# Optimization experiments

Hardware: AMD Instinct MI355X
Metric: run time of the kernel (lower is better)

## Reference

```python
import jax, jax.numpy as jnp
import numpy as np

V, E, HID, D = 10000, 512, 512, 14
FEAT = 512  # attention feature dim (== C)


def setup_inputs() -> dict:
    key = jax.random.key(0)
    ks = jax.random.split(key, 20)
    s = 0.02
    inp = {
        "features": jax.random.normal(ks[0], (32, 512, 7, 7), jnp.float32),
        "captions": jax.random.randint(ks[1], (32, 60), 0, V),
        "disease": jax.random.uniform(ks[2], (32, D), jnp.float32),
        # embedding
        "emb": jax.random.normal(ks[3], (V, E), jnp.float32) * s,
        # attention: attn Linear(feat+hid -> hid), v Linear(hid -> 1)
        "W_attn": jax.random.normal(ks[4], (FEAT + HID, HID), jnp.float32) * s,
        "b_attn": jnp.zeros((HID,), jnp.float32),
        "W_v": jax.random.normal(ks[5], (HID, 1), jnp.float32) * s,
        "b_v": jnp.zeros((1,), jnp.float32),
        # attention disease_proj: 14->128->512
        "W_dp1": jax.random.normal(ks[6], (D, 128), jnp.float32) * s,
        "b_dp1": jnp.zeros((128,), jnp.float32),
        "W_dp2": jax.random.normal(ks[7], (128, HID), jnp.float32) * s,
        "b_dp2": jnp.zeros((HID,), jnp.float32),
        # disease_encoder: 14->128->256 (dropout = identity at eval)
        "W_de1": jax.random.normal(ks[8], (D, 128), jnp.float32) * s,
        "b_de1": jnp.zeros((128,), jnp.float32),
        "W_de2": jax.random.normal(ks[9], (128, 256), jnp.float32) * s,
        "b_de2": jnp.zeros((256,), jnp.float32),
        # LSTM (input = E + 512 + 256 = 1280), gate order i,f,g,o
        "W_ih": jax.random.normal(ks[10], (E + FEAT + 256, 4 * HID), jnp.float32) * s,
        "W_hh": jax.random.normal(ks[11], (HID, 4 * HID), jnp.float32) * s,
        "b_ih": jnp.zeros((4 * HID,), jnp.float32),
        "b_hh": jnp.zeros((4 * HID,), jnp.float32),
        # fc: hid -> vocab
        "W_fc": jax.random.normal(ks[12], (HID, V), jnp.float32) * s,
        "b_fc": jnp.zeros((V,), jnp.float32),
    }
    return inp


def reference(features, captions, disease, emb, W_attn, b_attn, W_v, b_v,
              W_dp1, b_dp1, W_dp2, b_dp2, W_de1, b_de1, W_de2, b_de2,
              W_ih, W_hh, b_ih, b_hh, W_fc, b_fc):
    B, C = features.shape[0], features.shape[1]
    f = features.reshape(B, C, -1).transpose(0, 2, 1)  # [B, N, 512]

    embs = emb[captions]  # [B, T, E]

    # time-invariant disease contexts
    dis_ctx = jax.nn.relu(disease @ W_de1 + b_de1) @ W_de2 + b_de2   # [B,256]
    dis_att = jax.nn.relu(disease @ W_dp1 + b_dp1) @ W_dp2 + b_dp2  # [B,HID]

    # split attn weight: energy = tanh(f@Wf + (h+dis_att)@Wh + b)
    Wf, Wh = W_attn[:FEAT], W_attn[FEAT:]
    f_proj = jnp.einsum('bnf,fh->bnh', f, Wf)  # precompute feature part

    def step(carry, emb_t):
        h, c = carry  # [B,HID] each
        hid = h + dis_att
        energy = jnp.tanh(f_proj + (hid @ Wh + b_attn)[:, None, :])  # [B,N,HID]
        scores = (energy @ W_v).squeeze(-1) + b_v[0]                 # [B,N]
        alpha = jax.nn.softmax(scores, axis=1)
        context = jnp.einsum('bn,bnf->bf', alpha, f)                 # [B,512]
        x = jnp.concatenate([emb_t, context, dis_ctx], axis=1)       # [B,1280]
        gates = x @ W_ih + h @ W_hh + b_ih + b_hh
        i, fg, g, o = jnp.split(gates, 4, axis=1)
        c_new = jax.nn.sigmoid(fg) * c + jax.nn.sigmoid(i) * jnp.tanh(g)
        h_new = jax.nn.sigmoid(o) * jnp.tanh(c_new)
        return (h_new, c_new), h_new

    h0 = jnp.zeros((B, HID), f.dtype)
    c0 = jnp.zeros((B, HID), f.dtype)
    _, h_seq = jax.lax.scan(step, (h0, c0), embs.transpose(1, 0, 2))  # [T,B,HID]

    logits = h_seq @ W_fc + b_fc          # [T,B,V]
    return logits.transpose(1, 0, 2)      # [B,T,V]
```

## Files before the change

### kernel.cpp

```cpp
#include <hip/hip_runtime.h>
#include <math.h>

#define BB 32
#define NP 49
#define FE 512
#define HI 512
#define EM 512
#define TT 60
#define G4 2048
#define NV 10000
#define ND 14
#define NBLK 80

typedef __attribute__((ext_vector_type(8))) short short8v;
typedef __attribute__((ext_vector_type(4))) float float4v;

__device__ __forceinline__ float fsig(float x){ return 1.0f/(1.0f+__expf(-x)); }
__device__ __forceinline__ float ftanh(float x){
    x = fminf(fmaxf(x, -15.0f), 15.0f);
    float e = __expf(2.0f*x);
    return (e-1.0f)/(e+1.0f);
}
__device__ __forceinline__ ushort f2bf(float x){
    union { float f; unsigned u; } v; v.f = x;
    unsigned r = v.u + 0x7fff + ((v.u >> 16) & 1);
    return (ushort)(r >> 16);
}
__device__ __forceinline__ float bf2f(ushort h){
    union { float f; unsigned u; } v; v.u = ((unsigned)h) << 16;
    return v.f;
}
__device__ __forceinline__ ushort f2bf_trunc(float x){
    return (ushort)(__float_as_uint(x) >> 16);
}

__global__ void k_transpose(const float* __restrict__ feat, float* __restrict__ fT){
    int b = blockIdx.y;
    int cb = blockIdx.x * 64;
    __shared__ float tile[64][NP+1];
    const float* src = feat + (size_t)b*FE*NP;
    for (int idx = threadIdx.x; idx < 64*NP; idx += 256){
        int cl = idx / NP, n = idx % NP;
        tile[cl][n] = src[(size_t)(cb+cl)*NP + n];
    }
    __syncthreads();
    float* dst = fT + (size_t)b*NP*FE;
    for (int idx = threadIdx.x; idx < 64*NP; idx += 256){
        int cl = idx % 64, n = idx / 64;
        dst[(size_t)n*FE + cb + cl] = tile[cl][n];
    }
}

__global__ void k_disease(const float* __restrict__ dis,
                          const float* __restrict__ Wdp1, const float* __restrict__ bdp1,
                          const float* __restrict__ Wdp2, const float* __restrict__ bdp2,
                          const float* __restrict__ Wde1, const float* __restrict__ bde1,
                          const float* __restrict__ Wde2, const float* __restrict__ bde2,
                          const float* __restrict__ Wattn, const float* __restrict__ battn,
                          const float* __restrict__ Wih, const float* __restrict__ bih,
                          const float* __restrict__ bhh,
                          float* __restrict__ daw, float* __restrict__ disWih){
    int b = blockIdx.x;
    int tid = threadIdx.x;
    __shared__ float d[ND];
    __shared__ float hp[128], he[128];
    __shared__ float datt[HI];
    __shared__ float dctx[256];
    if (tid < ND) d[tid] = dis[b*ND + tid];
    __syncthreads();
    if (tid < 128){
        float accP = bdp1[tid], accE = bde1[tid];
        for (int k=0;k<ND;k++){ accP += d[k]*Wdp1[k*128+tid]; accE += d[k]*Wde1[k*128+tid]; }
        hp[tid] = fmaxf(accP, 0.f);
        he[tid] = fmaxf(accE, 0.f);
    }
    __syncthreads();
    for (int j = tid; j < HI; j += 256){
        float a = bdp2[j];
        for (int k=0;k<128;k++) a += hp[k]*Wdp2[k*HI+j];
        datt[j] = a;
    }
    if (tid < 256){
        float a = bde2[tid];
        for (int k=0;k<128;k++) a += he[k]*Wde2[k*256+tid];
        dctx[tid] = a;
    }
    __syncthreads();
    for (int j = tid; j < HI; j += 256){
        float a = battn[j];
        for (int k=0;k<HI;k++) a += datt[k]*Wattn[(size_t)(FE+k)*HI + j];
        daw[b*HI + j] = a;
    }
    for (int j = tid; j < G4; j += 256){
        float a = bih[j] + bhh[j];
        for (int k=0;k<256;k++) a += dctx[k]*Wih[(size_t)(EM+FE+k)*G4 + j];
        disWih[b*G4 + j] = a;
    }
}

__device__ __forceinline__ void stage_rows32(const float* __restrict__ src0, size_t ldsrc,
                                             const int* __restrict__ rowmap,
                                             ushort* h_hi, ushort* h_lo, int tid){
    #pragma unroll
    for (int it = 0; it < 4; it++){
        int flat = (it*512 + tid)*8;
        int row = flat >> 9, k = flat & 511;
        const float* src = src0 + (rowmap ? (size_t)rowmap[row]*ldsrc : (size_t)row*ldsrc) + k;
        float4 v0 = *(const float4*)(src);
        float4 v1 = *(const float4*)(src + 4);
        float fv[8] = {v0.x,v0.y,v0.z,v0.w,v1.x,v1.y,v1.z,v1.w};
        union { ushort u[8]; uint4 v; } ph, pl;
        #pragma unroll
        for (int j = 0; j < 8; j++){
            ushort hi = f2bf(fv[j]);
            ph.u[j] = hi;
            pl.u[j] = f2bf_trunc(fv[j] - bf2f(hi));
        }
        int di = (row*512 + k) ^ ((row&7)<<3);
        *(uint4*)&h_hi[di] = ph.v;
        *(uint4*)&h_lo[di] = pl.v;
    }
}

__device__ __forceinline__ void mfma_32x32(const ushort* h_hi, const ushort* h_lo,
                                           const float* __restrict__ Wb, size_t ldB, int col0,
                                           int lane, float4v acc[2][2]){
    int m = lane & 15, kg = lane >> 4;
    int a0 = m*512 + kg*8;
    int a1 = (16+m)*512 + kg*8;
    int axr = (m&7)<<3;
    for (int ks = 0; ks < 16; ks++){
        short8v ah0 = *(const short8v*)&h_hi[(a0 + ks*32) ^ axr];
        short8v al0 = *(const short8v*)&h_lo[(a0 + ks*32) ^ axr];
        short8v ah1 = *(const short8v*)&h_hi[(a1 + ks*32) ^ axr];
        short8v al1 = *(const short8v*)&h_lo[(a1 + ks*32) ^ axr];
        #pragma unroll
        for (int cj = 0; cj < 2; cj++){
            int v = col0 + cj*16 + m;
            int k0 = ks*32 + kg*8;
            const float* wp = Wb + (size_t)k0*ldB + v;
            float w[8];
            #pragma unroll
            for (int i = 0; i < 8; i++) w[i] = wp[(size_t)i*ldB];
            union { ushort u[8]; short8v s; } bh, bl;
            #pragma unroll
            for (int i = 0; i < 8; i++){
                ushort hi = f2bf(w[i]);
                bh.u[i] = hi;
                bl.u[i] = f2bf_trunc(w[i] - bf2f(hi));
            }
            acc[0][cj] = __builtin_amdgcn_mfma_f32_16x16x32_bf16(ah0, bh.s, acc[0][cj], 0,0,0);
            acc[0][cj] = __builtin_amdgcn_mfma_f32_16x16x32_bf16(al0, bh.s, acc[0][cj], 0,0,0);
            acc[0][cj] = __builtin_amdgcn_mfma_f32_16x16x32_bf16(ah0, bl.s, acc[0][cj], 0,0,0);
            acc[1][cj] = __builtin_amdgcn_mfma_f32_16x16x32_bf16(ah1, bh.s, acc[1][cj], 0,0,0);
            acc[1][cj] = __builtin_amdgcn_mfma_f32_16x16x32_bf16(al1, bh.s, acc[1][cj], 0,0,0);
            acc[1][cj] = __builtin_amdgcn_mfma_f32_16x16x32_bf16(ah1, bl.s, acc[1][cj], 0,0,0);
        }
    }
}

__launch_bounds__(512, 1)
__global__ void k_fproj(const float* __restrict__ fT, const float* __restrict__ Wattn,
                        float* __restrict__ f_proj){
    __shared__ __align__(16) ushort h_hi[16384], h_lo[16384];
    int r0 = blockIdx.x*32, vt = blockIdx.y;
    int tid = threadIdx.x, lane = tid & 63, wave = tid >> 6;
    stage_rows32(fT + (size_t)r0*FE, FE, nullptr, h_hi, h_lo, tid);
    __syncthreads();
    int col0 = vt*256 + wave*32;
    float4v acc[2][2];
    acc[0][0]=(float4v){0,0,0,0}; acc[0][1]=(float4v){0,0,0,0};
    acc[1][0]=(float4v){0,0,0,0}; acc[1][1]=(float4v){0,0,0,0};
    mfma_32x32(h_hi, h_lo, Wattn, HI, col0, lane, acc);
    int m = lane & 15, kg = lane >> 4;
    #pragma unroll
    for (int cj = 0; cj < 2; cj++){
        int col = col0 + cj*16 + m;
        #pragma unroll
        for (int ri = 0; ri < 2; ri++){
            int arow0 = ri*16 + kg*4;
            #pragma unroll
            for (int r = 0; r < 4; r++)
                f_proj[(size_t)(r0 + arow0 + r)*HI + col] = acc[ri][cj][r];
        }
    }
}

__launch_bounds__(512, 1)
__global__ void k_fwc(const float* __restrict__ fT, const float* __restrict__ Wih,
                      float* __restrict__ fWcP){
    __shared__ __align__(16) ushort h_hi[16384], h_lo[16384];
    int r0 = blockIdx.x*32, vt = blockIdx.y;
    int tid = threadIdx.x, lane = tid & 63, wave = tid >> 6;
    stage_rows32(fT + (size_t)r0*FE, FE, nullptr, h_hi, h_lo, tid);
    __syncthreads();
    int col0 = vt*256 + wave*32;
    float4v acc[2][2];
    acc[0][0]=(float4v){0,0,0,0}; acc[0][1]=(float4v){0,0,0,0};
    acc[1][0]=(float4v){0,0,0,0}; acc[1][1]=(float4v){0,0,0,0};
    mfma_32x32(h_hi, h_lo, Wih + (size_t)FE*G4, G4, col0, lane, acc);
    int m = lane & 15, kg = lane >> 4;
    #pragma unroll
    for (int cj = 0; cj < 2; cj++){
        int gc = col0 + cj*16 + m;
        int blk = (gc & 511) >> 3, m8 = gc & 7, g = gc >> 9;
        #pragma unroll
        for (int ri = 0; ri < 2; ri++){
            int arow0 = ri*16 + kg*4;
            #pragma unroll
            for (int r = 0; r < 4; r++){
                int R = r0 + arow0 + r;
                int b = R / 49, n = R - b*49;
                fWcP[(((size_t)blk*BB + b)*NP + n)*32 + m8*4 + g] = acc[ri][cj][r];
            }
        }
    }
}

__launch_bounds__(512, 1)
__global__ void k_preg(const int* __restrict__ caps, const float* __restrict__ emb,
                       const float* __restrict__ Wih, const float* __restrict__ disWih,
                       float* __restrict__ preGP){
    __shared__ __align__(16) ushort h_hi[16384], h_lo[16384];
    __shared__ int bidx[32];
    int r0 = blockIdx.x*32, vt = blockIdx.y;
    int tid = threadIdx.x, lane = tid & 63, wave = tid >> 6;
    if (tid < 32) bidx[tid] = caps[r0 + tid];
    __syncthreads();
    stage_rows32(emb, EM, bidx, h_hi, h_lo, tid);
    __syncthreads();
    int col0 = vt*256 + wave*32;
    float4v acc[2][2];
    acc[0][0]=(float4v){0,0,0,0}; acc[0][1]=(float4v){0,0,0,0};
    acc[1][0]=(float4v){0,0,0,0}; acc[1][1]=(float4v){0,0,0,0};
    mfma_32x32(h_hi, h_lo, Wih, G4, col0, lane, acc);
    int m = lane & 15, kg = lane >> 4;
    #pragma unroll
    for (int cj = 0; cj < 2; cj++){
        int gc = col0 + cj*16 + m;
        int blk = (gc & 511) >> 3, m8 = gc & 7, g = gc >> 9;
        #pragma unroll
        for (int ri = 0; ri < 2; ri++){
            int arow0 = ri*16 + kg*4;
            #pragma unroll
            for (int r = 0; r < 4; r++){
                int R = r0 + arow0 + r;
                int b = R / 60, t = R - b*60;
                preGP[(((size_t)blk*TT + t)*BB + b)*32 + m8*4 + g] =
                    acc[ri][cj][r] + disWih[b*G4 + gc];
            }
        }
    }
}

__device__ __forceinline__ void gridbar(int* bar, int tgt){
    __syncthreads();
    if (threadIdx.x == 0)
        __hip_atomic_store(bar + blockIdx.x, tgt, __ATOMIC_RELEASE, __HIP_MEMORY_SCOPE_AGENT);
    if (blockIdx.x == 0 && threadIdx.x < 64){
        int l = threadIdx.x;
        for (;;){
            int v0 = __hip_atomic_load(bar + l, __ATOMIC_RELAXED, __HIP_MEMORY_SCOPE_AGENT);
            int v1 = (l < NBLK-64) ? __hip_atomic_load(bar + 64 + l, __ATOMIC_RELAXED, __HIP_MEMORY_SCOPE_AGENT) : tgt;
            if (__all(v0 >= tgt && v1 >= tgt)) break;
            __builtin_amdgcn_s_sleep(1);
        }
        if (l == 0)
            __hip_atomic_store(bar + 128, tgt, __ATOMIC_RELEASE, __HIP_MEMORY_SCOPE_AGENT);
    }
    if (threadIdx.x == 0){
        while (__hip_atomic_load(bar + 128, __ATOMIC_RELAXED, __HIP_MEMORY_SCOPE_AGENT) < tgt)
            __builtin_amdgcn_s_sleep(1);
    }
    __syncthreads();
}

__launch_bounds__(512, 1)
__global__ void k_scan_coop(const float* __restrict__ f_proj, const float* __restrict__ fWcP,
                            const float* __restrict__ preGP, const float* __restrict__ daw,
                            const float* __restrict__ Wattn, const float* __restrict__ Whh,
                            const float* __restrict__ Wv,
                            float* __restrict__ h_seq, float* __restrict__ a_buf,
                            float* __restrict__ scores, int* __restrict__ bar){
    __shared__ __align__(16) ushort h_hi[16384], h_lo[16384];
    __shared__ __align__(16) ushort w_hi[16384], w_lo[16384];
    __shared__ float al[32*52];
    __shared__ float gbuf[32*33];
    __shared__ float daw_lds[32*32];
    __shared__ float gv[32*36];
    __shared__ float cst[256];
    __shared__ float wvl[512];
    int bk = blockIdx.x;
    int tid = threadIdx.x;
    int lane = tid & 63, wave = tid >> 6;
    bool isGate = bk < 64;

    {
        int k = tid;
        if (isGate){
            const float* wr = Whh + (size_t)k*G4 + bk*8;
            #pragma unroll
            for (int g = 0; g < 4; g++){
                float4 v0 = *(const float4*)(wr + g*512);
                float4 v1 = *(const float4*)(wr + g*512 + 4);
                float vv[8] = {v0.x,v0.y,v0.z,v0.w,v1.x,v1.y,v1.z,v1.w};
                #pragma unroll
                for (int u = 0; u < 8; u++){
                    int c = u*4 + g;
                    ushort hi = f2bf(vv[u]);
                    ushort lo = f2bf(vv[u] - bf2f(hi));
                    int idx = (c*512 + k) ^ ((c&7)<<3);
                    w_hi[idx] = hi; w_lo[idx] = lo;
                }
            }
        } else {
            const float* wr = Wattn + (size_t)(FE + k)*HI + (bk-64)*32;
            #pragma unroll
            for (int cq = 0; cq < 8; cq++){
                float4 v = *(const float4*)(wr + cq*4);
                float vv[4] = {v.x,v.y,v.z,v.w};
                #pragma unroll
                for (int q = 0; q < 4; q++){
                    int c = cq*4 + q;
                    ushort hi = f2bf(vv[q]);
                    ushort lo = f2bf(vv[q] - bf2f(hi));
                    int idx = (c*512 + k) ^ ((c&7)<<3);
                    w_hi[idx] = hi; w_lo[idx] = lo;
                }
            }
            for (int i = tid; i < 1024; i += 512){
                int b = i >> 5, c = i & 31;
                daw_lds[i] = daw[b*HI + (bk-64)*32 + c];
            }
        }
        if (tid < 256) cst[tid] = 0.f;
        wvl[tid] = Wv[tid];
    }
    __syncthreads();

    int tgt = 0;
    for (int t = 0; t < TT; t++){
        if (t == 0){
            uint4 z = make_uint4(0,0,0,0);
            #pragma unroll
            for (int it = 0; it < 4; it++){
                int flat = (it*512 + tid)*8;
                int b = flat >> 9, k = flat & 511;
                int di = (b*512 + k) ^ ((b&7)<<3);
                *(uint4*)&h_hi[di] = z;
                *(uint4*)&h_lo[di] = z;
            }
        } else {
            const float* hs = h_seq + (size_t)(t-1)*BB*HI;
            #pragma unroll
            for (int it = 0; it < 4; it++){
                int flat = (it*512 + tid)*8;
                int b = flat >> 9, k = flat & 511;
                float4 v0 = *(const float4*)(hs + flat);
                float4 v1 = *(const float4*)(hs + flat + 4);
                float fv[8] = {v0.x,v0.y,v0.z,v0.w,v1.x,v1.y,v1.z,v1.w};
                union { ushort u[8]; uint4 v; } ph, pl;
                #pragma unroll
                for (int j = 0; j < 8; j++){
                    ushort hi = f2bf(fv[j]);
                    ph.u[j] = hi;
                    pl.u[j] = f2bf(fv[j] - bf2f(hi));
                }
                int di = (b*512 + k) ^ ((b&7)<<3);
                *(uint4*)&h_hi[di] = ph.v;
                *(uint4*)&h_lo[di] = pl.v;
            }
        }
        __syncthreads();

        if (wave < 4){
            int rbase = (wave >> 1) * 16, cbase = (wave & 1) * 16;
            int m = lane & 15, kg = lane >> 4;
            int arow = rbase + m, bcol = cbase + m;
            int abase = arow*512 + kg*8, axr = (arow&7)<<3;
            int bbase = bcol*512 + kg*8, bxr = (bcol&7)<<3;
            float4v acc = {0.f,0.f,0.f,0.f};
            #pragma unroll
            for (int ks = 0; ks < 16; ks++){
                int ai = (abase + ks*32) ^ axr;
                int bi = (bbase + ks*32) ^ bxr;
                short8v ahi = *(const short8v*)&h_hi[ai];
                short8v alo = *(const short8v*)&h_lo[ai];
                short8v bhi = *(const short8v*)&w_hi[bi];
                short8v blo = *(const short8v*)&w_lo[bi];
                acc = __builtin_amdgcn_mfma_f32_16x16x32_bf16(ahi, bhi, acc, 0,0,0);
                acc = __builtin_amdgcn_mfma_f32_16x16x32_bf16(alo, bhi, acc, 0,0,0);
                acc = __builtin_amdgcn_mfma_f32_16x16x32_bf16(ahi, blo, acc, 0,0,0);
            }
            int ccol = cbase + (lane & 15);
            int crow0 = rbase + (lane >> 4)*4;
            if (isGate){
                #pragma unroll
                for (int r = 0; r < 4; r++)
                    gbuf[(crow0+r)*33 + ccol] = acc[r];
            } else {
                int cb = (bk-64)*32;
                float* ab = a_buf + (size_t)t*BB*HI;
                #pragma unroll
                for (int r = 0; r < 4; r++)
                    ab[(size_t)(crow0+r)*HI + cb + ccol] = acc[r] + daw_lds[(crow0+r)*32 + ccol];
            }
        }
        gridbar(bar, ++tgt);

        {
            int wid = tid >> 6, l = tid & 63;
            for (int p = bk + wid*NBLK; p < BB*NP; p += NBLK*8){
                int pb = p / NP, pn = p - pb*NP;
                const float* fpn = f_proj + ((size_t)pb*NP + pn)*HI;
                const float* at  = a_buf + ((size_t)t*BB + pb)*HI;
                int j = l*8;
                float4 f0 = *(const float4*)(fpn + j);
                float4 a0 = *(const float4*)(at + j);
                float4 f1 = *(const float4*)(fpn + j + 4);
                float4 a1 = *(const float4*)(at + j + 4);
                float s = wvl[j+0]*ftanh(f0.x + a0.x)
                        + wvl[j+1]*ftanh(f0.y + a0.y)
                        + wvl[j+2]*ftanh(f0.z + a0.z)
                        + wvl[j+3]*ftanh(f0.w + a0.w)
                        + wvl[j+4]*ftanh(f1.x + a1.x)
                        + wvl[j+5]*ftanh(f1.y + a1.y)
                        + wvl[j+6]*ftanh(f1.z + a1.z)
                        + wvl[j+7]*ftanh(f1.w + a1.w);
                #pragma unroll
                for (int off = 32; off; off >>= 1) s += __shfl_xor(s, off);
                if (l == 0) scores[t*(BB*NP) + p] = s;
            }
        }
        gridbar(bar, ++tgt);

        if (isGate){
            int hw = tid >> 5, l32 = tid & 31;
            #pragma unroll
            for (int rep = 0; rep < 2; rep++){
                int b = hw + rep*16;
                const float* sb = scores + t*(BB*NP) + b*NP;
                float s0 = sb[l32];
                float s1 = (l32 < 17) ? sb[32 + l32] : -1e30f;
                float m = fmaxf(s0, s1);
                #pragma unroll
                for (int off = 16; off; off >>= 1) m = fmaxf(m, __shfl_xor(m, off, 32));
                float e0 = __expf(s0 - m);
                float e1 = (l32 < 17) ? __expf(s1 - m) : 0.f;
                float sm = e0 + e1;
                #pragma unroll
                for (int off = 16; off; off >>= 1) sm += __shfl_xor(sm, off, 32);
                float inv = 1.f / sm;
                al[b*52 + l32] = e0*inv;
                if (l32 < 17) al[b*52 + 32 + l32] = e1*inv;
            }
            __syncthreads();
            {
                int b = tid >> 4, cp = tid & 15;
                float g0 = gbuf[b*33 + cp];
                float g1 = gbuf[b*33 + cp + 16];
                const float* pgp = preGP + (((size_t)bk*TT + t)*BB + b)*32;
                g0 += pgp[cp];
                g1 += pgp[cp + 16];
                const float* fw = fWcP + (((size_t)bk*BB + b)*NP)*32;
                for (int n = 0; n < NP; n++){
                    float av = al[b*52 + n];
                    g0 += av*fw[n*32 + cp];
                    g1 += av*fw[n*32 + cp + 16];
                }
                gv[b*36 + cp]      = g0;
                gv[b*36 + cp + 16] = g1;
            }
            __syncthreads();
            if (tid < 256){
                int b = tid >> 3, m = tid & 7;
                float gi = gv[b*36 + m*4 + 0];
                float gf = gv[b*36 + m*4 + 1];
                float gg = gv[b*36 + m*4 + 2];
                float go = gv[b*36 + m*4 + 3];
                float cn = fsig(gf)*cst[b*8 + m] + fsig(gi)*ftanh(gg);
                float hn = fsig(go)*ftanh(cn);
                cst[b*8 + m] = cn;
                h_seq[(size_t)t*BB*HI + b*HI + bk*8 + m] = hn;
            }
        }
        gridbar(bar, ++tgt);
    }
}

__launch_bounds__(512, 1)
__global__ void k_logits(const float* __restrict__ h_seq, const float* __restrict__ Wfc,
                         const float* __restrict__ bfc, float* __restrict__ out){
    __shared__ __align__(16) ushort h_hi[16384], h_lo[16384];
    int t = blockIdx.x, vt = blockIdx.y;
    int tid = threadIdx.x, lane = tid & 63, wave = tid >> 6;
    stage_rows32(h_seq + (size_t)t*BB*HI, HI, nullptr, h_hi, h_lo, tid);
    __syncthreads();

    int m = lane & 15, kg = lane >> 4;
    int cb = vt*256 + wave*32;
    int a0 = m*512 + kg*8;
    int a1 = (16+m)*512 + kg*8;
    int axr = (m&7)<<3;
    float4v acc[2][2];
    acc[0][0]=(float4v){0,0,0,0}; acc[0][1]=(float4v){0,0,0,0};
    acc[1][0]=(float4v){0,0,0,0}; acc[1][1]=(float4v){0,0,0,0};
    const short8v bz = {0,0,0,0,0,0,0,0};

    for (int ks = 0; ks < 16; ks++){
        short8v ah0 = *(const short8v*)&h_hi[(a0 + ks*32) ^ axr];
        short8v al0 = *(const short8v*)&h_lo[(a0 + ks*32) ^ axr];
        short8v ah1 = *(const short8v*)&h_hi[(a1 + ks*32) ^ axr];
        short8v al1 = *(const short8v*)&h_lo[(a1 + ks*32) ^ axr];
        #pragma unroll
        for (int cj = 0; cj < 2; cj++){
            int v = cb + cj*16 + m;
            short8v bhi = bz, blo = bz;
            if (v < NV){
                int k0 = ks*32 + kg*8;
                const float* wp = Wfc + (size_t)k0*NV + v;
                float w[8];
                #pragma unroll
                for (int i = 0; i < 8; i++) w[i] = wp[(size_t)i*NV];
                union { ushort u[8]; short8v s; } bh, bl;
                #pragma unroll
                for (int i = 0; i < 8; i++){
                    ushort hi = f2bf(w[i]);
                    bh.u[i] = hi;
                    bl.u[i] = f2bf_trunc(w[i] - bf2f(hi));
                }
                bhi = bh.s; blo = bl.s;
            }
            acc[0][cj] = __builtin_amdgcn_mfma_f32_16x16x32_bf16(ah0, bhi, acc[0][cj], 0,0,0);
            acc[0][cj] = __builtin_amdgcn_mfma_f32_16x16x32_bf16(al0, bhi, acc[0][cj], 0,0,0);
            acc[0][cj] = __builtin_amdgcn_mfma_f32_16x16x32_bf16(ah0, blo, acc[0][cj], 0,0,0);
            acc[1][cj] = __builtin_amdgcn_mfma_f32_16x16x32_bf16(ah1, bhi, acc[1][cj], 0,0,0);
            acc[1][cj] = __builtin_amdgcn_mfma_f32_16x16x32_bf16(al1, bhi, acc[1][cj], 0,0,0);
            acc[1][cj] = __builtin_amdgcn_mfma_f32_16x16x32_bf16(ah1, blo, acc[1][cj], 0,0,0);
        }
    }
    #pragma unroll
    for (int cj = 0; cj < 2; cj++){
        int v = cb + cj*16 + m;
        if (v < NV){
            float bias = bfc[v];
            #pragma unroll
            for (int ri = 0; ri < 2; ri++){
                int b0 = ri*16 + kg*4;
                #pragma unroll
                for (int r = 0; r < 4; r++)
                    out[((size_t)(b0+r)*TT + t)*NV + v] = acc[ri][cj][r] + bias;
            }
        }
    }
}

extern "C" void kernel_launch(void* const* d_in, const int* in_sizes, int n_in,
                              void* d_out, int out_size, void* d_ws, size_t ws_size,
                              hipStream_t stream){
    const float* features = (const float*)d_in[0];
    const int*   captions = (const int*)d_in[1];
    const float* disease  = (const float*)d_in[2];
    const float* emb      = (const float*)d_in[3];
    const float* W_attn   = (const float*)d_in[4];
    const float* b_attn   = (const float*)d_in[5];
    const float* W_v      = (const float*)d_in[6];
    const float* W_dp1    = (const float*)d_in[8];
    const float* b_dp1    = (const float*)d_in[9];
    const float* W_dp2    = (const float*)d_in[10];
    const float* b_dp2    = (const float*)d_in[11];
    const float* W_de1    = (const float*)d_in[12];
    const float* b_de1    = (const float*)d_in[13];
    const float* W_de2    = (const float*)d_in[14];
    const float* b_de2    = (const float*)d_in[15];
    const float* W_ih     = (const float*)d_in[16];
    const float* W_hh     = (const float*)d_in[17];
    const float* b_ih     = (const float*)d_in[18];
    const float* b_hh     = (const float*)d_in[19];
    const float* W_fc     = (const float*)d_in[20];
    const float* b_fc     = (const float*)d_in[21];
    float* out = (float*)d_out;

    const size_t N_HSEQ = (size_t)TT*BB*HI;
    float* h_seq = (float*)d_ws;
    int*   bar   = (int*)((char*)d_ws + N_HSEQ*sizeof(float));

    const size_t N_FT   = (size_t)BB*NP*FE;
    const size_t N_FP   = (size_t)BB*NP*HI;
    const size_t N_FWC  = (size_t)BB*NP*G4;
    const size_t N_PREG = (size_t)BB*TT*G4;
    const size_t N_ABUF = (size_t)TT*BB*HI;
    const size_t N_SC   = (size_t)TT*BB*NP;
    float* fT     = out;
    float* f_proj = fT + N_FT;
    float* fWcP   = f_proj + N_FP;
    float* preGP  = fWcP + N_FWC;
    float* a_buf  = preGP + N_PREG;
    float* scores = a_buf + N_ABUF;
    float* disWih = scores + N_SC;
    float* daw    = disWih + (size_t)BB*G4;

    hipMemsetAsync(bar, 0, 1024, stream);
    k_transpose<<<dim3(8,BB),256,0,stream>>>(features, fT);
    k_disease<<<BB,256,0,stream>>>(disease, W_dp1,b_dp1,W_dp2,b_dp2,
                                   W_de1,b_de1,W_de2,b_de2,
                                   W_attn,b_attn, W_ih,b_ih,b_hh,
                                   daw, disWih);
    k_fproj<<<dim3(49,2),512,0,stream>>>(fT, W_attn, f_proj);
    k_fwc<<<dim3(49,8),512,0,stream>>>(fT, W_ih, fWcP);
    k_preg<<<dim3(60,8),512,0,stream>>>(captions, emb, W_ih, disWih, preGP);
    k_scan_coop<<<NBLK,512,0,stream>>>(f_proj, fWcP, preGP, daw,
                                       W_attn, W_hh, W_v,
                                       h_seq, a_buf, scores, bar);
    k_logits<<<dim3(TT,40),512,0,stream>>>(h_seq, W_fc, b_fc, out);
}
```

Baseline: 1.668 ms.

## Pad grid-barrier flags to separate cache lines and process two timesteps per logits block

The grid barrier now stores each block's arrival flag 64 bytes apart, and the release flag is fanned out to ten padded copies, each polled by a group of eight blocks. This is meant to cut false sharing and polling contention during the 60 sequential scan steps. Separately, the logits kernel now handles two timesteps (64 rows) per block, so each bf16-split W_fc tile is loaded and converted once for twice as many MFMAs. The cost is doubled LDS and accumulator use and half as many blocks in the logits grid.

Result: no change. 1.693 ms (+1.5%).

```diff
diff --git a/kernel.cpp b/kernel.cpp
--- a/kernel.cpp
+++ b/kernel.cpp
@@ -256,20 +256,21 @@
 __device__ __forceinline__ void gridbar(int* bar, int tgt){
     __syncthreads();
     if (threadIdx.x == 0)
-        __hip_atomic_store(bar + blockIdx.x, tgt, __ATOMIC_RELEASE, __HIP_MEMORY_SCOPE_AGENT);
+        __hip_atomic_store(bar + blockIdx.x*16, tgt, __ATOMIC_RELEASE, __HIP_MEMORY_SCOPE_AGENT);
     if (blockIdx.x == 0 && threadIdx.x < 64){
         int l = threadIdx.x;
         for (;;){
-            int v0 = __hip_atomic_load(bar + l, __ATOMIC_RELAXED, __HIP_MEMORY_SCOPE_AGENT);
-            int v1 = (l < NBLK-64) ? __hip_atomic_load(bar + 64 + l, __ATOMIC_RELAXED, __HIP_MEMORY_SCOPE_AGENT) : tgt;
+            int v0 = __hip_atomic_load(bar + l*16, __ATOMIC_RELAXED, __HIP_MEMORY_SCOPE_AGENT);
+            int v1 = (l < NBLK-64) ? __hip_atomic_load(bar + (64+l)*16, __ATOMIC_RELAXED, __HIP_MEMORY_SCOPE_AGENT) : tgt;
             if (__all(v0 >= tgt && v1 >= tgt)) break;
             __builtin_amdgcn_s_sleep(1);
         }
-        if (l == 0)
-            __hip_atomic_store(bar + 128, tgt, __ATOMIC_RELEASE, __HIP_MEMORY_SCOPE_AGENT);
+        if (l < 10)
+            __hip_atomic_store(bar + 1536 + l*16, tgt, __ATOMIC_RELEASE, __HIP_MEMORY_SCOPE_AGENT);
     }
     if (threadIdx.x == 0){
-        while (__hip_atomic_load(bar + 128, __ATOMIC_RELAXED, __HIP_MEMORY_SCOPE_AGENT) < tgt)
+        int g = blockIdx.x >> 3;
+        while (__hip_atomic_load(bar + 1536 + g*16, __ATOMIC_RELAXED, __HIP_MEMORY_SCOPE_AGENT) < tgt)
             __builtin_amdgcn_s_sleep(1);
     }
     __syncthreads();
@@ -491,27 +492,49 @@
 __launch_bounds__(512, 1)
 __global__ void k_logits(const float* __restrict__ h_seq, const float* __restrict__ Wfc,
                          const float* __restrict__ bfc, float* __restrict__ out){
-    __shared__ __align__(16) ushort h_hi[16384], h_lo[16384];
-    int t = blockIdx.x, vt = blockIdx.y;
+    __shared__ __align__(16) ushort h_hi[32768], h_lo[32768];
+    int t0 = blockIdx.x*2, vt = blockIdx.y;
     int tid = threadIdx.x, lane = tid & 63, wave = tid >> 6;
-    stage_rows32(h_seq + (size_t)t*BB*HI, HI, nullptr, h_hi, h_lo, tid);
+    const float* hs = h_seq + (size_t)t0*BB*HI;
+    #pragma unroll
+    for (int it = 0; it < 8; it++){
+        int flat = (it*512 + tid)*8;
+        int row = flat >> 9, k = flat & 511;
+        float4 v0 = *(const float4*)(hs + flat);
+        float4 v1 = *(const float4*)(hs + flat + 4);
+        float fv[8] = {v0.x,v0.y,v0.z,v0.w,v1.x,v1.y,v1.z,v1.w};
+        union { ushort u[8]; uint4 v; } ph, pl;
+        #pragma unroll
+        for (int j = 0; j < 8; j++){
+            ushort hi = f2bf(fv[j]);
+            ph.u[j] = hi;
+            pl.u[j] = f2bf_trunc(fv[j] - bf2f(hi));
+        }
+        int di = (row*512 + k) ^ ((row&7)<<3);
+        *(uint4*)&h_hi[di] = ph.v;
+        *(uint4*)&h_lo[di] = pl.v;
+    }
     __syncthreads();
 
     int m = lane & 15, kg = lane >> 4;
     int cb = vt*256 + wave*32;
-    int a0 = m*512 + kg*8;
-    int a1 = (16+m)*512 + kg*8;
+    int ab[4];
+    #pragma unroll
+    for (int rg = 0; rg < 4; rg++) ab[rg] = (rg*16 + m)*512 + kg*8;
     int axr = (m&7)<<3;
-    float4v acc[2][2];
-    acc[0][0]=(float4v){0,0,0,0}; acc[0][1]=(float4v){0,0,0,0};
-    acc[1][0]=(float4v){0,0,0,0}; acc[1][1]=(float4v){0,0,0,0};
+    float4v acc[4][2];
+    #pragma unroll
+    for (int rg = 0; rg < 4; rg++){ acc[rg][0]=(float4v){0,0,0,0}; acc[rg][1]=(float4v){0,0,0,0}; }
     const short8v bz = {0,0,0,0,0,0,0,0};
 
     for (int ks = 0; ks < 16; ks++){
-        short8v ah0 = *(const short8v*)&h_hi[(a0 + ks*32) ^ axr];
-        short8v al0 = *(const short8v*)&h_lo[(a0 + ks*32) ^ axr];
-        short8v ah1 = *(const short8v*)&h_hi[(a1 + ks*32) ^ axr];
-        short8v al1 = *(const short8v*)&h_lo[(a1 + ks*32) ^ axr];
+        short8v ah[4], al[4];
+        #pragma unroll
+        for (int rg = 0; rg < 4; rg++){
+            int ai = (ab[rg] + ks*32) ^ axr;
+            ah[rg] = *(const short8v*)&h_hi[ai];
+            al[rg] = *(const short8v*)&h_lo[ai];
+        }
         #pragma unroll
         for (int cj = 0; cj < 2; cj++){
             int v = cb + cj*16 + m;
@@ -531,12 +554,12 @@
                 }
                 bhi = bh.s; blo = bl.s;
             }
-            acc[0][cj] = __builtin_amdgcn_mfma_f32_16x16x32_bf16(ah0, bhi, acc[0][cj], 0,0,0);
-            acc[0][cj] = __builtin_amdgcn_mfma_f32_16x16x32_bf16(al0, bhi, acc[0][cj], 0,0,0);
-            acc[0][cj] = __builtin_amdgcn_mfma_f32_16x16x32_bf16(ah0, blo, acc[0][cj], 0,0,0);
-            acc[1][cj] = __builtin_amdgcn_mfma_f32_16x16x32_bf16(ah1, bhi, acc[1][cj], 0,0,0);
-            acc[1][cj] = __builtin_amdgcn_mfma_f32_16x16x32_bf16(al1, bhi, acc[1][cj], 0,0,0);
-            acc[1][cj] = __builtin_amdgcn_mfma_f32_16x16x32_bf16(ah1, blo, acc[1][cj], 0,0,0);
+            #pragma unroll
+            for (int rg = 0; rg < 4; rg++){
+                acc[rg][cj] = __builtin_amdgcn_mfma_f32_16x16x32_bf16(ah[rg], bhi, acc[rg][cj], 0,0,0);
+                acc[rg][cj] = __builtin_amdgcn_mfma_f32_16x16x32_bf16(al[rg], bhi, acc[rg][cj], 0,0,0);
+                acc[rg][cj] = __builtin_amdgcn_mfma_f32_16x16x32_bf16(ah[rg], blo, acc[rg][cj], 0,0,0);
+            }
         }
     }
     #pragma unroll
@@ -545,11 +568,12 @@
         if (v < NV){
             float bias = bfc[v];
             #pragma unroll
-            for (int ri = 0; ri < 2; ri++){
-                int b0 = ri*16 + kg*4;
+            for (int rg = 0; rg < 4; rg++){
+                int t = t0 + (rg >> 1);
+                int b0 = (rg & 1)*16 + kg*4;
                 #pragma unroll
                 for (int r = 0; r < 4; r++)
-                    out[((size_t)(b0+r)*TT + t)*NV + v] = acc[ri][cj][r] + bias;
+                    out[((size_t)(b0+r)*TT + t)*NV + v] = acc[rg][cj][r] + bias;
             }
         }
     }
@@ -600,7 +624,7 @@
     float* disWih = scores + N_SC;
     float* daw    = disWih + (size_t)BB*G4;
 
-    hipMemsetAsync(bar, 0, 1024, stream);
+    hipMemsetAsync(bar, 0, 8192, stream);
     k_transpose<<<dim3(8,BB),256,0,stream>>>(features, fT);
     k_disease<<<BB,256,0,stream>>>(disease, W_dp1,b_dp1,W_dp2,b_dp2,
                                    W_de1,b_de1,W_de2,b_de2,
@@ -612,5 +636,5 @@
     k_scan_coop<<<NBLK,512,0,stream>>>(f_proj, fWcP, preGP, daw,
                                        W_attn, W_hh, W_v,
                                        h_seq, a_buf, scores, bar);
-    k_logits<<<dim3(TT,40),512,0,stream>>>(h_seq, W_fc, b_fc, out);
-}
+    k_logits<<<dim3(TT/2,40),512,0,stream>>>(h_seq, W_fc, b_fc, out);
+}
```
